# Optimization experiments

Hardware: AMD Instinct MI355X
Metric: run time of the kernel (lower is better)

Reference implementation:

```python
import jax, jax.numpy as jnp
import numpy as np

N, C, M, P, FL = 2, 512, 8, 1, 4
SPATIAL = [(100, 100), (50, 50), (25, 25), (13, 13)]
S = sum(h * w for h, w in SPATIAL)
CM = C // M


def grid_sample_zeros(im, grid):
    """torch.nn.functional.grid_sample, bilinear, padding_mode='zeros', align_corners=False.
    im: (B, Cc, H, W); grid: (B, Hg, Wg, 2) with grid[...,0]=x, grid[...,1]=y in [-1,1].
    Returns (B, Cc, Hg, Wg)."""
    B, Cc, H, W = im.shape
    Hg, Wg = grid.shape[1], grid.shape[2]
    x = (grid[..., 0] + 1.0) * (W * 0.5) - 0.5
    y = (grid[..., 1] + 1.0) * (H * 0.5) - 0.5
    x0f = jnp.floor(x)
    y0f = jnp.floor(y)
    wx1 = x - x0f
    wy1 = y - y0f
    wx0 = 1.0 - wx1
    wy0 = 1.0 - wy1
    x0 = x0f.astype(jnp.int32)
    y0 = y0f.astype(jnp.int32)
    flat = im.reshape(B, Cc, H * W)

    def gather(ix, iy):
        valid = ((ix >= 0) & (ix < W) & (iy >= 0) & (iy < H)).astype(im.dtype)
        idx = jnp.clip(iy, 0, H - 1) * W + jnp.clip(ix, 0, W - 1)  # (B,Hg,Wg)
        idx = jnp.broadcast_to(idx.reshape(B, 1, Hg * Wg), (B, Cc, Hg * Wg))
        v = jnp.take_along_axis(flat, idx, axis=2).reshape(B, Cc, Hg, Wg)
        return v * valid[:, None]

    out = (gather(x0, y0) * (wx0 * wy0)[:, None]
           + gather(x0 + 1, y0) * (wx1 * wy0)[:, None]
           + gather(x0, y0 + 1) * (wx0 * wy1)[:, None]
           + gather(x0 + 1, y0 + 1) * (wx1 * wy1)[:, None])
    return out


def setup_inputs() -> dict:
    key = jax.random.key(0)
    ks = jax.random.split(key, 8)
    x = jax.random.normal(ks[0], (N, C, S), jnp.float32)
    pos = jax.random.normal(ks[1], (N, C, S), jnp.float32)
    key_padding_mask = jnp.zeros((N, S), jnp.bool_)
    # valid (W,H) per level; no padding -> full size, scale 1
    valid_sizes = jnp.broadcast_to(
        jnp.array([[w, h] for (h, w) in SPATIAL], jnp.float32)[None], (N, FL, 2))
    valid_scales = jnp.ones((N, FL, 2), jnp.float32)
    s = 1.0 / np.sqrt(C)
    Wv = (jax.random.normal(ks[2], (C, C), jnp.float32) * s)
    bv = jnp.zeros((C,), jnp.float32)
    Wloc = jax.random.normal(ks[3], (M * FL * P * 2, C), jnp.float32) * 0.01
    # torch bias init: head-direction grid, channel layout (M, F, P, 2)
    grid_init = np.array([-1, -1, -1, 0, -1, 1, 0, -1, 0, 1, 1, -1, 1, 0, 1, 1],
                         np.float32).reshape(M, 1, 1, 2)
    grid_init = np.tile(grid_init, (1, FL, P, 1))
    for i in range(P):
        grid_init[:, :, i, :] *= (i + 1)
    bloc = jnp.asarray(grid_init.reshape(-1))
    Ww = jax.random.normal(ks[4], (M * FL * P, C), jnp.float32) * 0.01
    bw = jnp.zeros((M * FL * P,), jnp.float32)
    Wo = (jax.random.normal(ks[5], (C, C), jnp.float32) * s)
    bo = jnp.zeros((C,), jnp.float32)
    scale = jnp.ones((C,), jnp.float32)
    return dict(x=x, pos=pos, key_padding_mask=key_padding_mask,
                valid_sizes=valid_sizes, valid_scales=valid_scales,
                Wv=Wv, bv=bv, Wloc=Wloc, bloc=bloc, Ww=Ww, bw=bw,
                Wo=Wo, bo=bo, scale=scale)


def reference(x, pos, key_padding_mask, valid_sizes, valid_scales,
              Wv, bv, Wloc, bloc, Ww, bw, Wo, bo, scale):
    mask = key_padding_mask[:, None, :]  # (N,1,S)
    x_pos = jnp.where(mask, 0.0, x + pos)
    value = jnp.einsum('oc,ncs->nos', Wv, x) + bv[:, None]
    value = jnp.where(mask, 0.0, value)

    # per-level value maps, split heads: (N*M, C/M, H, W)
    values, cur = [], 0
    for (H, W) in SPATIAL:
        values.append(value[..., cur:cur + H * W].reshape(N * M, CM, H, W))
        cur += H * W

    vs = jnp.repeat(valid_sizes, M, axis=0)          # (NM, F, 2) = repeat_interleave
    vc2 = jnp.repeat(2.0 * valid_scales, M, axis=0)  # (NM, F, 2)

    outs, cur = [], 0
    for lvl, (H, W) in enumerate(SPATIAL):
        L = H * W
        xp = x_pos[..., cur:cur + L]  # (N, C, L)
        cur += L
        # 1x1 convs == per-token linears
        off = jnp.einsum('oc,ncl->nol', Wloc, xp) + bloc[:, None]
        off = off.reshape(N * M, FL, P, 2, L).transpose(0, 1, 2, 4, 3)  # (NM,F,P,L,2)
        w = jnp.einsum('oc,ncl->nol', Ww, xp) + bw[:, None]
        w = jax.nn.softmax(w.reshape(N * M, 1, FL * P, L), axis=2)
        # pixel-center grid of the query level, (L,2) as (x,y)
        ys, xs = jnp.meshgrid(jnp.arange(H, dtype=jnp.float32) + 0.5,
                              jnp.arange(W, dtype=jnp.float32) + 0.5, indexing='ij')
        pre = jnp.stack([xs, ys], -1).reshape(L, 2)
        sc = (vc2 / vs[:, lvl:lvl + 1])[:, :, None, None, :]  # (NM,F,1,1,2)
        grids = off * sc + (pre[None, None, None] * sc - 1.0)  # (NM,F,P,L,2)
        samples = jnp.concatenate(
            [grid_sample_zeros(values[f], grids[:, f]) for f in range(FL)], axis=2)  # (NM,CM,F*P,L)
        out = jnp.sum(samples * w, axis=2).reshape(N, C, L)
        out = jnp.einsum('oc,ncl->nol', Wo, out) + bo[:, None]
        outs.append(out)
    return jnp.concatenate(outs, axis=-1) * scale[None, :, None]
```

## Files before the change

kernel.cpp:

```cpp
#include <hip/hip_runtime.h>
#include <math.h>

#define TOT_S   13294
#define NBATCH  2
#define CCH     512
#define MHEAD   8
#define PITCH   40

typedef short     short8  __attribute__((ext_vector_type(8)));
typedef float     f32x4   __attribute__((ext_vector_type(4)));
typedef unsigned short u16x8 __attribute__((ext_vector_type(8)));
typedef unsigned short u16x4 __attribute__((ext_vector_type(4)));

__device__ __forceinline__ unsigned short f2bf(float f) {
    union { float f; unsigned int u; } v; v.f = f;
    unsigned int r = v.u + 0x7fffu + ((v.u >> 16) & 1u);
    return (unsigned short)(r >> 16);
}
__device__ __forceinline__ float bf2f(unsigned short h) {
    union { unsigned int u; float f; } v; v.u = ((unsigned int)h) << 16;
    return v.f;
}

__global__ void cast_f32_bf16(const float* __restrict__ src,
                              unsigned short* __restrict__ dst, int n4)
{
    const int i = blockIdx.x * blockDim.x + threadIdx.x;
    if (i < n4) {
        const float4 v = *(const float4*)(src + (size_t)i * 4);
        u16x4 o;
        o[0] = f2bf(v.x); o[1] = f2bf(v.y); o[2] = f2bf(v.z); o[3] = f2bf(v.w);
        *(u16x4*)(dst + (size_t)i * 4) = o;
    }
}

__global__ __launch_bounds__(512)
void gemm_value_mfma(const unsigned short* __restrict__ Wb,
                     const float* __restrict__ x,
                     const float* __restrict__ bv,
                     const unsigned char* __restrict__ mask,
                     unsigned short* __restrict__ valb)
{
    __shared__ unsigned short Wl[2][128 * PITCH];
    __shared__ unsigned short Al[2][128 * PITCH];
    const int n  = blockIdx.z;
    const int ob = blockIdx.y * 128;
    const int sb = blockIdx.x * 128;
    const int tid = threadIdx.x;

    const int r   = tid >> 2;
    const int seg = (tid & 3) * 8;
    const unsigned short* wsrc = Wb + ((size_t)(ob + r)) * CCH + seg;

    const int sp   = tid & 15;
    const int cgrp = (tid >> 4) & 15;
    const int half = tid >> 8;
    const size_t XLIM = (size_t)NBATCH * CCH * TOT_S - 2;

    const int wave = tid >> 6, lane = tid & 63;
    const int m0 = (wave & 1) * 64, n0 = (wave >> 1) * 32;
    const int row16 = lane & 15, q = lane >> 4;

    u16x8 w0 = *(const u16x8*)(wsrc);
    float2 ax[2][2];
#pragma unroll
    for (int cc = 0; cc < 2; ++cc)
#pragma unroll
        for (int jj = 0; jj < 2; ++jj) {
            size_t off = ((size_t)n * CCH + 2 * cgrp + cc) * TOT_S
                       + sb + 2 * sp + 32 * (2 * half + jj);
            off = off > XLIM ? XLIM : off;
            ax[cc][jj] = *(const float2*)(x + off);
        }
    *(u16x8*)&Wl[0][r * PITCH + seg] = w0;
#pragma unroll
    for (int jj = 0; jj < 2; ++jj)
#pragma unroll
        for (int i = 0; i < 2; ++i) {
            const int s = 2 * sp + 32 * (2 * half + jj) + i;
            const float lo = i ? ax[0][jj].y : ax[0][jj].x;
            const float hi = i ? ax[1][jj].y : ax[1][jj].x;
            *(unsigned int*)&Al[0][(size_t)s * PITCH + 2 * cgrp] =
                (unsigned int)f2bf(lo) | ((unsigned int)f2bf(hi) << 16);
        }
    __syncthreads();

    f32x4 acc[4][2] = {};
    int cur = 0;
    for (int k0 = 0; k0 < CCH; k0 += 32) {
        const bool more = (k0 + 32) < CCH;
        u16x8 wn = {};
        float2 axn[2][2];
        if (more) {
            wn = *(const u16x8*)(wsrc + k0 + 32);
#pragma unroll
            for (int cc = 0; cc < 2; ++cc)
#pragma unroll
                for (int jj = 0; jj < 2; ++jj) {
                    size_t off = ((size_t)n * CCH + k0 + 32 + 2 * cgrp + cc) * TOT_S
                               + sb + 2 * sp + 32 * (2 * half + jj);
                    off = off > XLIM ? XLIM : off;
                    axn[cc][jj] = *(const float2*)(x + off);
                }
        }
        short8 af[4], bfr[2];
#pragma unroll
        for (int mt = 0; mt < 4; ++mt)
            af[mt] = *(const short8*)&Wl[cur][(m0 + mt * 16 + row16) * PITCH + q * 8];
#pragma unroll
        for (int nt = 0; nt < 2; ++nt)
            bfr[nt] = *(const short8*)&Al[cur][(n0 + nt * 16 + row16) * PITCH + q * 8];
#pragma unroll
        for (int mt = 0; mt < 4; ++mt)
#pragma unroll
            for (int nt = 0; nt < 2; ++nt)
                acc[mt][nt] = __builtin_amdgcn_mfma_f32_16x16x32_bf16(
                    af[mt], bfr[nt], acc[mt][nt], 0, 0, 0);
        if (more) {
            *(u16x8*)&Wl[cur ^ 1][r * PITCH + seg] = wn;
#pragma unroll
            for (int jj = 0; jj < 2; ++jj)
#pragma unroll
                for (int i = 0; i < 2; ++i) {
                    const int s = 2 * sp + 32 * (2 * half + jj) + i;
                    const float lo = i ? axn[0][jj].y : axn[0][jj].x;
                    const float hi = i ? axn[1][jj].y : axn[1][jj].x;
                    *(unsigned int*)&Al[cur ^ 1][(size_t)s * PITCH + 2 * cgrp] =
                        (unsigned int)f2bf(lo) | ((unsigned int)f2bf(hi) << 16);
                }
        }
        __syncthreads();
        cur ^= 1;
    }

#pragma unroll
    for (int nt = 0; nt < 2; ++nt) {
        const int s = sb + n0 + nt * 16 + row16;
        if (s >= TOT_S) continue;
        const float msk = mask[(size_t)n * TOT_S + s] ? 0.f : 1.f;
        unsigned short* orow = valb + ((size_t)n * TOT_S + s) * CCH + ob + m0;
#pragma unroll
        for (int mt = 0; mt < 4; ++mt) {
            const f32x4 bvv = *(const f32x4*)(bv + ob + m0 + mt * 16 + q * 4);
            const f32x4 a = acc[mt][nt];
            u16x4 ov;
            ov[0] = f2bf((a[0] + bvv[0]) * msk);
            ov[1] = f2bf((a[1] + bvv[1]) * msk);
            ov[2] = f2bf((a[2] + bvv[2]) * msk);
            ov[3] = f2bf((a[3] + bvv[3]) * msk);
            *(u16x4*)(orow + mt * 16 + q * 4) = ov;
        }
    }
}

__global__ __launch_bounds__(256)
void gemm_offw_mfma(const unsigned short* __restrict__ Wlb,
                    const unsigned short* __restrict__ Wwb,
                    const float* __restrict__ bloc, const float* __restrict__ bw,
                    const float* __restrict__ x, const float* __restrict__ pos,
                    const unsigned char* __restrict__ mask,
                    float* __restrict__ offw)
{
    __shared__ unsigned short Wl[128 * PITCH];
    __shared__ unsigned short Al[128 * PITCH];
    const int n  = blockIdx.z;
    const int sb = blockIdx.x * 128;
    const int tid = threadIdx.x;

    const int r   = tid >> 1;
    const int seg = (tid & 1) * 16;
    const bool wzero = (r >= 96);
    const unsigned short* wsrc =
        (r < 64) ? (Wlb + (size_t)r * CCH + seg)
                 : (Wwb + (size_t)((r < 96 ? r : 95) - 64) * CCH + seg);
    unsigned short* wdst = &Wl[r * PITCH + seg];

    const int sp   = tid & 15;
    const int cpid = tid >> 4;
    const size_t XLIM = (size_t)NBATCH * CCH * TOT_S - 2;
    float mkm[8];
#pragma unroll
    for (int j = 0; j < 4; ++j)
#pragma unroll
        for (int i = 0; i < 2; ++i) {
            const int s = sb + 2 * sp + 32 * j + i;
            const int sc = s < TOT_S ? s : TOT_S - 1;
            mkm[j * 2 + i] = mask[(size_t)n * TOT_S + sc] ? 0.f : 1.f;
        }

    const int wave = tid >> 6, lane = tid & 63;
    const int m0 = (wave & 1) * 64, n0 = (wave >> 1) * 64;
    const int row16 = lane & 15, q = lane >> 4;

    u16x8 w0 = {}, w1 = {};
    if (!wzero) { w0 = *(const u16x8*)(wsrc); w1 = *(const u16x8*)(wsrc + 8); }
    float2 ax[2][4], ap[2][4];
#pragma unroll
    for (int cc = 0; cc < 2; ++cc)
#pragma unroll
        for (int j = 0; j < 4; ++j) {
            size_t off = ((size_t)n * CCH + 2 * cpid + cc) * TOT_S
                       + sb + 2 * sp + 32 * j;
            off = off > XLIM ? XLIM : off;
            ax[cc][j] = *(const float2*)(x + off);
            ap[cc][j] = *(const float2*)(pos + off);
        }

    f32x4 acc[4][4] = {};
    for (int k0 = 0; k0 < CCH; k0 += 32) {
        *(u16x8*)wdst = w0; *(u16x8*)(wdst + 8) = w1;
#pragma unroll
        for (int j = 0; j < 4; ++j)
#pragma unroll
            for (int i = 0; i < 2; ++i) {
                const int s = 2 * sp + 32 * j + i;
                const float lo = (i ? ax[0][j].y + ap[0][j].y
                                    : ax[0][j].x + ap[0][j].x) * mkm[j * 2 + i];
                const float hi = (i ? ax[1][j].y + ap[1][j].y
                                    : ax[1][j].x + ap[1][j].x) * mkm[j * 2 + i];
                const unsigned int pk =
                    (unsigned int)f2bf(lo) | ((unsigned int)f2bf(hi) << 16);
                *(unsigned int*)&Al[(size_t)s * PITCH + 2 * cpid] = pk;
            }
        __syncthreads();
        if (k0 + 32 < CCH) {
            if (!wzero) {
                w0 = *(const u16x8*)(wsrc + k0 + 32);
                w1 = *(const u16x8*)(wsrc + k0 + 40);
            }
#pragma unroll
            for (int cc = 0; cc < 2; ++cc)
#pragma unroll
                for (int j = 0; j < 4; ++j) {
                    size_t off = ((size_t)n * CCH + k0 + 32 + 2 * cpid + cc) * TOT_S
                               + sb + 2 * sp + 32 * j;
                    off = off > XLIM ? XLIM : off;
                    ax[cc][j] = *(const float2*)(x + off);
                    ap[cc][j] = *(const float2*)(pos + off);
                }
        }
        short8 af[4], bfr[4];
#pragma unroll
        for (int mt = 0; mt < 4; ++mt)
            af[mt] = *(const short8*)&Wl[(m0 + mt * 16 + row16) * PITCH + q * 8];
#pragma unroll
        for (int nt = 0; nt < 4; ++nt)
            bfr[nt] = *(const short8*)&Al[(n0 + nt * 16 + row16) * PITCH + q * 8];
#pragma unroll
        for (int mt = 0; mt < 4; ++mt)
#pragma unroll
            for (int nt = 0; nt < 4; ++nt)
                acc[mt][nt] = __builtin_amdgcn_mfma_f32_16x16x32_bf16(
                    af[mt], bfr[nt], acc[mt][nt], 0, 0, 0);
        __syncthreads();
    }

#pragma unroll
    for (int nt = 0; nt < 4; ++nt) {
        const int s = sb + n0 + nt * 16 + row16;
        if (s >= TOT_S) continue;
        float* orow = offw + ((size_t)n * TOT_S + s) * 96;
#pragma unroll
        for (int mt = 0; mt < 4; ++mt) {
            const int o = m0 + mt * 16 + q * 4;
            if (o < 96) {
                const float* bsrc = (o < 64) ? (bloc + o) : (bw + o - 64);
                const f32x4 bb = *(const f32x4*)bsrc;
                f32x4 v = acc[mt][nt];
                v[0] += bb[0]; v[1] += bb[1]; v[2] += bb[2]; v[3] += bb[3];
                *(f32x4*)(orow + o) = v;
            }
        }
    }
}

__global__ __launch_bounds__(256)
void sample_attn(const unsigned short* __restrict__ value,
                 const float* __restrict__ offw,
                 const float* __restrict__ vsizes,
                 const float* __restrict__ vscales,
                 unsigned short* __restrict__ samp)
{
    const int lane = threadIdx.x;
    const int item = blockIdx.x * blockDim.y + threadIdx.y;
    const int total = NBATCH * TOT_S;
    if (item >= total) return;
    const int s = item % TOT_S;
    const int n = item / TOT_S;
    const int m = lane >> 3;

    int lvl; float prex, prey;
    if (s < 10000)      { lvl = 0; const int l = s;         const int qq = l / 100; prey = qq + 0.5f; prex = (l - qq * 100) + 0.5f; }
    else if (s < 12500) { lvl = 1; const int l = s - 10000; const int qq = l / 50;  prey = qq + 0.5f; prex = (l - qq * 50)  + 0.5f; }
    else if (s < 13125) { lvl = 2; const int l = s - 12500; const int qq = l / 25;  prey = qq + 0.5f; prex = (l - qq * 25)  + 0.5f; }
    else                { lvl = 3; const int l = s - 13125; const int qq = l / 13;  prey = qq + 0.5f; prex = (l - qq * 13)  + 0.5f; }

    const float* ow = offw + ((size_t)n * TOT_S + s) * 96;

    const float w0 = ow[64 + m * 4 + 0], w1 = ow[64 + m * 4 + 1];
    const float w2 = ow[64 + m * 4 + 2], w3 = ow[64 + m * 4 + 3];
    const float mx = fmaxf(fmaxf(w0, w1), fmaxf(w2, w3));
    const float e0 = expf(w0 - mx), e1 = expf(w1 - mx), e2 = expf(w2 - mx), e3 = expf(w3 - mx);
    const float inv = 1.f / (e0 + e1 + e2 + e3);
    const float wgt[4] = { e0 * inv, e1 * inv, e2 * inv, e3 * inv };

    const int HS[4]  = { 100, 50, 25, 13 };
    const int WS[4]  = { 100, 50, 25, 13 };
    const int CUR[4] = { 0, 10000, 12500, 13125 };

    const float invsx = 1.f / vsizes[((n * 4) + lvl) * 2 + 0];
    const float invsy = 1.f / vsizes[((n * 4) + lvl) * 2 + 1];
    const unsigned short* vbase = value + (size_t)n * TOT_S * CCH + lane * 8;

    float acc[8] = {};
#pragma unroll
    for (int f = 0; f < 4; ++f) {
        const float offx = ow[(m * 4 + f) * 2 + 0];
        const float offy = ow[(m * 4 + f) * 2 + 1];
        const float scx = 2.f * vscales[((n * 4) + f) * 2 + 0] * invsx;
        const float scy = 2.f * vscales[((n * 4) + f) * 2 + 1] * invsy;
        const int Wf = WS[f], Hf = HS[f], cf = CUR[f];
        const float xi = (offx + prex) * scx * (Wf * 0.5f) - 0.5f;
        const float yi = (offy + prey) * scy * (Hf * 0.5f) - 0.5f;
        const float x0f = floorf(xi), y0f = floorf(yi);
        const float wx1 = xi - x0f, wy1 = yi - y0f;
        const float wx0 = 1.f - wx1, wy0 = 1.f - wy1;
        const int x0 = (int)x0f, y0 = (int)y0f;
        const bool xin0 = (x0 >= 0) && (x0 < Wf);
        const bool xin1 = (x0 + 1 >= 0) && (x0 + 1 < Wf);
        const bool yin0 = (y0 >= 0) && (y0 < Hf);
        const bool yin1 = (y0 + 1 >= 0) && (y0 + 1 < Hf);
        const float cw00 = (xin0 && yin0) ? wgt[f] * wx0 * wy0 : 0.f;
        const float cw10 = (xin1 && yin0) ? wgt[f] * wx1 * wy0 : 0.f;
        const float cw01 = (xin0 && yin1) ? wgt[f] * wx0 * wy1 : 0.f;
        const float cw11 = (xin1 && yin1) ? wgt[f] * wx1 * wy1 : 0.f;
        const int x0c = min(max(x0, 0), Wf - 1);
        const int x1c = min(max(x0 + 1, 0), Wf - 1);
        const int y0c = min(max(y0, 0), Hf - 1);
        const int y1c = min(max(y0 + 1, 0), Hf - 1);
        const unsigned short* row0 = vbase + (size_t)(cf + y0c * Wf) * CCH;
        const unsigned short* row1 = vbase + (size_t)(cf + y1c * Wf) * CCH;
        const u16x8 v00 = *(const u16x8*)(row0 + (size_t)x0c * CCH);
        const u16x8 v10 = *(const u16x8*)(row0 + (size_t)x1c * CCH);
        const u16x8 v01 = *(const u16x8*)(row1 + (size_t)x0c * CCH);
        const u16x8 v11 = *(const u16x8*)(row1 + (size_t)x1c * CCH);
#pragma unroll
        for (int j = 0; j < 8; ++j) {
            acc[j] += cw00 * bf2f(v00[j]) + cw10 * bf2f(v10[j])
                    + cw01 * bf2f(v01[j]) + cw11 * bf2f(v11[j]);
        }
    }

    u16x8 ov;
#pragma unroll
    for (int j = 0; j < 8; ++j) ov[j] = f2bf(acc[j]);
    *(u16x8*)(samp + ((size_t)n * TOT_S + s) * CCH + lane * 8) = ov;
}

__global__ __launch_bounds__(512)
void gemm_out_mfma(const unsigned short* __restrict__ Wob,
                   const unsigned short* __restrict__ Sampb,
                   const float* __restrict__ bo, const float* __restrict__ scale,
                   float* __restrict__ out)
{
    __shared__ unsigned short Sl[2][128 * PITCH];
    __shared__ unsigned short Wl[2][128 * PITCH];
    const int n  = blockIdx.z;
    const int ob = blockIdx.y * 128;
    const int sb = blockIdx.x * 128;
    const int tid = threadIdx.x;
    const int r   = tid >> 2;
    const int seg = (tid & 3) * 8;
    const int sr = min(sb + r, TOT_S - 1);
    const unsigned short* ssrc = Sampb + ((size_t)n * TOT_S + sr) * CCH + seg;
    const unsigned short* wsrc = Wob + ((size_t)(ob + r)) * CCH + seg;

    const int wave = tid >> 6, lane = tid & 63;
    const int m0 = (wave & 1) * 64, n0 = (wave >> 1) * 32;
    const int row16 = lane & 15, q = lane >> 4;

    u16x8 s0v = *(const u16x8*)(ssrc);
    u16x8 w0v = *(const u16x8*)(wsrc);
    *(u16x8*)&Sl[0][r * PITCH + seg] = s0v;
    *(u16x8*)&Wl[0][r * PITCH + seg] = w0v;
    __syncthreads();

    f32x4 acc[4][2] = {};
    int cur = 0;
    for (int k0 = 0; k0 < CCH; k0 += 32) {
        const bool more = (k0 + 32) < CCH;
        u16x8 sn = {}, wn = {};
        if (more) {
            sn = *(const u16x8*)(ssrc + k0 + 32);
            wn = *(const u16x8*)(wsrc + k0 + 32);
        }
        short8 af[4], bfr[2];
#pragma unroll
        for (int mt = 0; mt < 4; ++mt)
            af[mt] = *(const short8*)&Sl[cur][(m0 + mt * 16 + row16) * PITCH + q * 8];
#pragma unroll
        for (int nt = 0; nt < 2; ++nt)
            bfr[nt] = *(const short8*)&Wl[cur][(n0 + nt * 16 + row16) * PITCH + q * 8];
#pragma unroll
        for (int mt = 0; mt < 4; ++mt)
#pragma unroll
            for (int nt = 0; nt < 2; ++nt)
                acc[mt][nt] = __builtin_amdgcn_mfma_f32_16x16x32_bf16(
                    af[mt], bfr[nt], acc[mt][nt], 0, 0, 0);
        if (more) {
            *(u16x8*)&Sl[cur ^ 1][r * PITCH + seg] = sn;
            *(u16x8*)&Wl[cur ^ 1][r * PITCH + seg] = wn;
        }
        __syncthreads();
        cur ^= 1;
    }

#pragma unroll
    for (int nt = 0; nt < 2; ++nt) {
        const int o = ob + n0 + nt * 16 + row16;
        const float bo_ = bo[o];
        const float sc_ = scale[o];
        float* orow = out + ((size_t)n * CCH + o) * (size_t)TOT_S;
#pragma unroll
        for (int mt = 0; mt < 4; ++mt) {
            const int s0 = sb + m0 + mt * 16 + q * 4;
            const f32x4 a = acc[mt][nt];
            if (s0 + 3 < TOT_S) {
                float2 v0 = make_float2((a[0] + bo_) * sc_, (a[1] + bo_) * sc_);
                float2 v1 = make_float2((a[2] + bo_) * sc_, (a[3] + bo_) * sc_);
                *(float2*)(orow + s0) = v0;
                *(float2*)(orow + s0 + 2) = v1;
            } else {
                for (int i = 0; i < 4; ++i)
                    if (s0 + i < TOT_S) orow[s0 + i] = (a[i] + bo_) * sc_;
            }
        }
    }
}

extern "C" void kernel_launch(void* const* d_in, const int* in_sizes, int n_in,
                              void* d_out, int out_size, void* d_ws, size_t ws_size,
                              hipStream_t stream)
{
    const float* x     = (const float*)d_in[0];
    const float* pos   = (const float*)d_in[1];
    const unsigned char* mask = (const unsigned char*)d_in[2];
    const float* vsz   = (const float*)d_in[3];
    const float* vsc   = (const float*)d_in[4];
    const float* Wv    = (const float*)d_in[5];
    const float* bv    = (const float*)d_in[6];
    const float* Wloc  = (const float*)d_in[7];
    const float* bloc  = (const float*)d_in[8];
    const float* Ww    = (const float*)d_in[9];
    const float* bw    = (const float*)d_in[10];
    const float* Wo    = (const float*)d_in[11];
    const float* bo    = (const float*)d_in[12];
    const float* scale = (const float*)d_in[13];
    float* out = (float*)d_out;

    const size_t SC = (size_t)TOT_S * CCH;
    unsigned short* valb  = (unsigned short*)d_ws;
    unsigned short* sampb = valb  + 2 * SC;
    float* offw = (float*)(sampb + 2 * SC);
    unsigned short* wvb = (unsigned short*)(offw + 2 * (size_t)TOT_S * 96);
    unsigned short* wob = wvb + 512 * 512;
    unsigned short* wlb = wob + 512 * 512;
    unsigned short* wwb = wlb + 64 * 512;

    cast_f32_bf16<<<256, 256, 0, stream>>>(Wv,   wvb, 512 * 512 / 4);
    cast_f32_bf16<<<256, 256, 0, stream>>>(Wo,   wob, 512 * 512 / 4);
    cast_f32_bf16<<<32,  256, 0, stream>>>(Wloc, wlb, 64 * 512 / 4);
    cast_f32_bf16<<<16,  256, 0, stream>>>(Ww,   wwb, 32 * 512 / 4);

    const int sTiles = (TOT_S + 127) / 128;

    gemm_value_mfma<<<dim3(sTiles, CCH / 128, NBATCH), 512, 0, stream>>>(
        wvb, x, bv, mask, valb);
    gemm_offw_mfma<<<dim3(sTiles, 1, NBATCH), 256, 0, stream>>>(
        wlb, wwb, bloc, bw, x, pos, mask, offw);

    const int items = NBATCH * TOT_S;
    sample_attn<<<(items + 3) / 4, dim3(64, 4), 0, stream>>>(valb, offw, vsz, vsc, sampb);

    gemm_out_mfma<<<dim3(sTiles, CCH / 128, NBATCH), 512, 0, stream>>>(
        wob, sampb, bo, scale, out);
}
```

Measured before the change: 290.9 us.

## Stage 64-wide K tiles per barrier pair in both projection GEMMs

Both MFMA GEMMs (value projection and output projection) now load 64 channels of K per iteration into two 32-wide LDS halves, where before they double-buffered one 32-wide tile. The goal is to halve the number of loop iterations and barriers while keeping register prefetch of the next 64-wide tile overlapped with the MFMA work. The cost is two barriers per iteration instead of one, more prefetch registers per thread, and no LDS double buffering, so the LDS writes can no longer overlap the previous tile's compute.

```diff
diff --git a/kernel.cpp b/kernel.cpp
--- a/kernel.cpp
+++ b/kernel.cpp
@@ -48,9 +48,11 @@
     const int sb = blockIdx.x * 128;
     const int tid = threadIdx.x;
 
-    const int r   = tid >> 2;
-    const int seg = (tid & 3) * 8;
-    const unsigned short* wsrc = Wb + ((size_t)(ob + r)) * CCH + seg;
+    const int r    = tid >> 2;
+    const int wh   = (tid & 3) >> 1;
+    const int segh = (tid & 1) * 16;
+    const unsigned short* wsrc = Wb + ((size_t)(ob + r)) * CCH + wh * 32 + segh;
+    unsigned short* wdst = &Wl[wh][r * PITCH + segh];
 
     const int sp   = tid & 15;
     const int cgrp = (tid >> 4) & 15;
@@ -62,75 +64,69 @@
     const int row16 = lane & 15, q = lane >> 4;
 
     u16x8 w0 = *(const u16x8*)(wsrc);
-    float2 ax[2][2];
-#pragma unroll
-    for (int cc = 0; cc < 2; ++cc)
-#pragma unroll
-        for (int jj = 0; jj < 2; ++jj) {
-            size_t off = ((size_t)n * CCH + 2 * cgrp + cc) * TOT_S
-                       + sb + 2 * sp + 32 * (2 * half + jj);
-            off = off > XLIM ? XLIM : off;
-            ax[cc][jj] = *(const float2*)(x + off);
-        }
-    *(u16x8*)&Wl[0][r * PITCH + seg] = w0;
-#pragma unroll
-    for (int jj = 0; jj < 2; ++jj)
-#pragma unroll
-        for (int i = 0; i < 2; ++i) {
-            const int s = 2 * sp + 32 * (2 * half + jj) + i;
-            const float lo = i ? ax[0][jj].y : ax[0][jj].x;
-            const float hi = i ? ax[1][jj].y : ax[1][jj].x;
-            *(unsigned int*)&Al[0][(size_t)s * PITCH + 2 * cgrp] =
-                (unsigned int)f2bf(lo) | ((unsigned int)f2bf(hi) << 16);
-        }
-    __syncthreads();
+    u16x8 w1 = *(const u16x8*)(wsrc + 8);
+    float2 ax[2][2][2];
+#pragma unroll
+    for (int kh = 0; kh < 2; ++kh)
+#pragma unroll
+        for (int cc = 0; cc < 2; ++cc)
+#pragma unroll
+            for (int jj = 0; jj < 2; ++jj) {
+                size_t off = ((size_t)n * CCH + kh * 32 + 2 * cgrp + cc) * TOT_S
+                           + sb + 2 * sp + 32 * (2 * half + jj);
+                off = off > XLIM ? XLIM : off;
+                ax[kh][cc][jj] = *(const float2*)(x + off);
+            }
 
     f32x4 acc[4][2] = {};
-    int cur = 0;
-    for (int k0 = 0; k0 < CCH; k0 += 32) {
-        const bool more = (k0 + 32) < CCH;
-        u16x8 wn = {};
-        float2 axn[2][2];
-        if (more) {
-            wn = *(const u16x8*)(wsrc + k0 + 32);
-#pragma unroll
-            for (int cc = 0; cc < 2; ++cc)
-#pragma unroll
-                for (int jj = 0; jj < 2; ++jj) {
-                    size_t off = ((size_t)n * CCH + k0 + 32 + 2 * cgrp + cc) * TOT_S
-                               + sb + 2 * sp + 32 * (2 * half + jj);
-                    off = off > XLIM ? XLIM : off;
-                    axn[cc][jj] = *(const float2*)(x + off);
-                }
-        }
-        short8 af[4], bfr[2];
-#pragma unroll
-        for (int mt = 0; mt < 4; ++mt)
-            af[mt] = *(const short8*)&Wl[cur][(m0 + mt * 16 + row16) * PITCH + q * 8];
-#pragma unroll
-        for (int nt = 0; nt < 2; ++nt)
-            bfr[nt] = *(const short8*)&Al[cur][(n0 + nt * 16 + row16) * PITCH + q * 8];
-#pragma unroll
-        for (int mt = 0; mt < 4; ++mt)
-#pragma unroll
-            for (int nt = 0; nt < 2; ++nt)
-                acc[mt][nt] = __builtin_amdgcn_mfma_f32_16x16x32_bf16(
-                    af[mt], bfr[nt], acc[mt][nt], 0, 0, 0);
-        if (more) {
-            *(u16x8*)&Wl[cur ^ 1][r * PITCH + seg] = wn;
+    for (int k0 = 0; k0 < CCH; k0 += 64) {
+        *(u16x8*)wdst = w0; *(u16x8*)(wdst + 8) = w1;
+#pragma unroll
+        for (int kh = 0; kh < 2; ++kh)
 #pragma unroll
             for (int jj = 0; jj < 2; ++jj)
 #pragma unroll
                 for (int i = 0; i < 2; ++i) {
                     const int s = 2 * sp + 32 * (2 * half + jj) + i;
-                    const float lo = i ? axn[0][jj].y : axn[0][jj].x;
-                    const float hi = i ? axn[1][jj].y : axn[1][jj].x;
-                    *(unsigned int*)&Al[cur ^ 1][(size_t)s * PITCH + 2 * cgrp] =
+                    const float lo = i ? ax[kh][0][jj].y : ax[kh][0][jj].x;
+                    const float hi = i ? ax[kh][1][jj].y : ax[kh][1][jj].x;
+                    *(unsigned int*)&Al[kh][(size_t)s * PITCH + 2 * cgrp] =
                         (unsigned int)f2bf(lo) | ((unsigned int)f2bf(hi) << 16);
                 }
-        }
-        __syncthreads();
-        cur ^= 1;
+        __syncthreads();
+        if (k0 + 64 < CCH) {
+            w0 = *(const u16x8*)(wsrc + k0 + 64);
+            w1 = *(const u16x8*)(wsrc + k0 + 72);
+#pragma unroll
+            for (int kh = 0; kh < 2; ++kh)
+#pragma unroll
+                for (int cc = 0; cc < 2; ++cc)
+#pragma unroll
+                    for (int jj = 0; jj < 2; ++jj) {
+                        size_t off = ((size_t)n * CCH + k0 + 64 + kh * 32
+                                      + 2 * cgrp + cc) * TOT_S
+                                   + sb + 2 * sp + 32 * (2 * half + jj);
+                        off = off > XLIM ? XLIM : off;
+                        ax[kh][cc][jj] = *(const float2*)(x + off);
+                    }
+        }
+#pragma unroll
+        for (int kh = 0; kh < 2; ++kh) {
+            short8 af[4], bfr[2];
+#pragma unroll
+            for (int mt = 0; mt < 4; ++mt)
+                af[mt] = *(const short8*)&Wl[kh][(m0 + mt * 16 + row16) * PITCH + q * 8];
+#pragma unroll
+            for (int nt = 0; nt < 2; ++nt)
+                bfr[nt] = *(const short8*)&Al[kh][(n0 + nt * 16 + row16) * PITCH + q * 8];
+#pragma unroll
+            for (int mt = 0; mt < 4; ++mt)
+#pragma unroll
+                for (int nt = 0; nt < 2; ++nt)
+                    acc[mt][nt] = __builtin_amdgcn_mfma_f32_16x16x32_bf16(
+                        af[mt], bfr[nt], acc[mt][nt], 0, 0, 0);
+        }
+        __syncthreads();
     }
 
 #pragma unroll
@@ -369,50 +365,52 @@
     const int ob = blockIdx.y * 128;
     const int sb = blockIdx.x * 128;
     const int tid = threadIdx.x;
-    const int r   = tid >> 2;
-    const int seg = (tid & 3) * 8;
+    const int r    = tid >> 2;
+    const int wh   = (tid & 3) >> 1;
+    const int segh = (tid & 1) * 16;
     const int sr = min(sb + r, TOT_S - 1);
-    const unsigned short* ssrc = Sampb + ((size_t)n * TOT_S + sr) * CCH + seg;
-    const unsigned short* wsrc = Wob + ((size_t)(ob + r)) * CCH + seg;
+    const unsigned short* ssrc = Sampb + ((size_t)n * TOT_S + sr) * CCH + wh * 32 + segh;
+    const unsigned short* wsrc = Wob + ((size_t)(ob + r)) * CCH + wh * 32 + segh;
+    unsigned short* sdst = &Sl[wh][r * PITCH + segh];
+    unsigned short* wdst = &Wl[wh][r * PITCH + segh];
 
     const int wave = tid >> 6, lane = tid & 63;
     const int m0 = (wave & 1) * 64, n0 = (wave >> 1) * 32;
     const int row16 = lane & 15, q = lane >> 4;
 
     u16x8 s0v = *(const u16x8*)(ssrc);
+    u16x8 s1v = *(const u16x8*)(ssrc + 8);
     u16x8 w0v = *(const u16x8*)(wsrc);
-    *(u16x8*)&Sl[0][r * PITCH + seg] = s0v;
-    *(u16x8*)&Wl[0][r * PITCH + seg] = w0v;
-    __syncthreads();
+    u16x8 w1v = *(const u16x8*)(wsrc + 8);
 
     f32x4 acc[4][2] = {};
-    int cur = 0;
-    for (int k0 = 0; k0 < CCH; k0 += 32) {
-        const bool more = (k0 + 32) < CCH;
-        u16x8 sn = {}, wn = {};
-        if (more) {
-            sn = *(const u16x8*)(ssrc + k0 + 32);
-            wn = *(const u16x8*)(wsrc + k0 + 32);
-        }
-        short8 af[4], bfr[2];
-#pragma unroll
-        for (int mt = 0; mt < 4; ++mt)
-            af[mt] = *(const short8*)&Sl[cur][(m0 + mt * 16 + row16) * PITCH + q * 8];
-#pragma unroll
-        for (int nt = 0; nt < 2; ++nt)
-            bfr[nt] = *(const short8*)&Wl[cur][(n0 + nt * 16 + row16) * PITCH + q * 8];
-#pragma unroll
-        for (int mt = 0; mt < 4; ++mt)
+    for (int k0 = 0; k0 < CCH; k0 += 64) {
+        *(u16x8*)sdst = s0v; *(u16x8*)(sdst + 8) = s1v;
+        *(u16x8*)wdst = w0v; *(u16x8*)(wdst + 8) = w1v;
+        __syncthreads();
+        if (k0 + 64 < CCH) {
+            s0v = *(const u16x8*)(ssrc + k0 + 64);
+            s1v = *(const u16x8*)(ssrc + k0 + 72);
+            w0v = *(const u16x8*)(wsrc + k0 + 64);
+            w1v = *(const u16x8*)(wsrc + k0 + 72);
+        }
+#pragma unroll
+        for (int kh = 0; kh < 2; ++kh) {
+            short8 af[4], bfr[2];
+#pragma unroll
+            for (int mt = 0; mt < 4; ++mt)
+                af[mt] = *(const short8*)&Sl[kh][(m0 + mt * 16 + row16) * PITCH + q * 8];
 #pragma unroll
             for (int nt = 0; nt < 2; ++nt)
-                acc[mt][nt] = __builtin_amdgcn_mfma_f32_16x16x32_bf16(
-                    af[mt], bfr[nt], acc[mt][nt], 0, 0, 0);
-        if (more) {
-            *(u16x8*)&Sl[cur ^ 1][r * PITCH + seg] = sn;
-            *(u16x8*)&Wl[cur ^ 1][r * PITCH + seg] = wn;
-        }
-        __syncthreads();
-        cur ^= 1;
+                bfr[nt] = *(const short8*)&Wl[kh][(n0 + nt * 16 + row16) * PITCH + q * 8];
+#pragma unroll
+            for (int mt = 0; mt < 4; ++mt)
+#pragma unroll
+                for (int nt = 0; nt < 2; ++nt)
+                    acc[mt][nt] = __builtin_amdgcn_mfma_f32_16x16x32_bf16(
+                        af[mt], bfr[nt], acc[mt][nt], 0, 0, 0);
+        }
+        __syncthreads();
     }
 
 #pragma unroll
```

After: 287.7 us. No clear change (-1.1%).
